# Performance work log

Measured on AMD Instinct MI355X. Metric: run time of the kernel, lower is better.

The kernel has to match this reference:

```python
import jax, jax.numpy as jnp
import numpy as np

N_NODES = 100000
D = 256
N_TYPES = 4
E1 = 300000
E2 = 300000


def setup_inputs() -> dict:
    key = jax.random.key(0)
    ks = jax.random.split(key, 9)
    x = jax.random.normal(ks[0], (N_NODES, D), dtype=jnp.float32)
    hyperedge_index_s1 = jax.random.randint(ks[1], (2, E1 * 1), 0, N_NODES, dtype=jnp.int32)
    hyperedge_type_s1 = jax.random.randint(ks[2], (E1,), 0, N_TYPES, dtype=jnp.int32)
    hyperedge_index_s2 = jax.random.randint(ks[3], (2, E2 * 2), 0, N_NODES, dtype=jnp.int32)
    hyperedge_type_s2 = jax.random.randint(ks[4], (E2,), 0, N_TYPES, dtype=jnp.int32)
    # xavier_normal init for A: std = sqrt(2 / (fan_in + fan_out))
    A_s1 = jax.random.normal(ks[5], (N_TYPES, 1 * D, D), dtype=jnp.float32) * np.sqrt(2.0 / (D + D)).astype(np.float32)
    A_s2 = jax.random.normal(ks[6], (N_TYPES, 2 * D, D), dtype=jnp.float32) * np.sqrt(2.0 / (2 * D + D)).astype(np.float32)
    lim = 1.0 / np.sqrt(D)
    W_c = jax.random.uniform(ks[7], (D, D), minval=-lim, maxval=lim, dtype=jnp.float32)
    b_c = jax.random.uniform(ks[8], (D,), minval=-lim, maxval=lim, dtype=jnp.float32)
    return dict(x=x,
                hyperedge_index_s1=hyperedge_index_s1, hyperedge_type_s1=hyperedge_type_s1,
                hyperedge_index_s2=hyperedge_index_s2, hyperedge_type_s2=hyperedge_type_s2,
                A_s1=A_s1, A_s2=A_s2, W_c=W_c, b_c=b_c)


def _shape_agg(x, A, idx, etype, shape, n_nodes):
    """Per-hyperedge-shape gather -> per-type matmul -> normalize -> scatter-add."""
    d = x.shape[1]
    e = etype.shape[0]
    # concat the `shape` source node features per hyperedge: [E, shape*d]
    src = x[idx[0]].reshape(e, shape * d)
    # first target slot per hyperedge: [E]
    dst = idx[1].reshape(e, shape)[:, 0]
    agg = jnp.zeros((n_nodes, d), dtype=x.dtype)
    for t in range(A.shape[0]):  # small fixed number of edge types
        mask = etype == t
        tmp = src @ A[t]  # [E, d]
        # per-destination count within this (shape, type) group == torch.unique counts
        counts = jax.ops.segment_sum(mask.astype(x.dtype), dst, num_segments=n_nodes)
        norm = jnp.where(mask, 1.0 / jnp.maximum(counts[dst], 1.0), 0.0)
        agg = agg.at[dst].add(norm[:, None] * tmp)
    return agg


def reference(x, hyperedge_index_s1, hyperedge_type_s1,
              hyperedge_index_s2, hyperedge_type_s2,
              A_s1, A_s2, W_c, b_c):
    n = x.shape[0]
    agg = _shape_agg(x, A_s1, hyperedge_index_s1, hyperedge_type_s1, 1, n)
    agg = agg + _shape_agg(x, A_s2, hyperedge_index_s2, hyperedge_type_s2, 2, n)
    return x @ W_c.T + b_c + agg
```

## Files before the change

### kernel.cpp

```cpp
#include <hip/hip_runtime.h>
#include <stdint.h>

#define N_NODES 100000
#define D 256
#define NT 4

typedef float f32x4 __attribute__((ext_vector_type(4)));
typedef __bf16 bf16x8 __attribute__((ext_vector_type(8)));
typedef unsigned int uint32x4 __attribute__((ext_vector_type(4)));
typedef unsigned int uint32x2 __attribute__((ext_vector_type(2)));

__device__ __forceinline__ unsigned short f2bf(float f) {
    unsigned u = __float_as_uint(f);
    u += 0x7FFF + ((u >> 16) & 1);
    return (unsigned short)(u >> 16);
}

__device__ __forceinline__ void gload_lds16(const void* g, void* lds) {
    __builtin_amdgcn_global_load_lds(
        (const __attribute__((address_space(1))) unsigned int*)g,
        (__attribute__((address_space(3))) unsigned int*)lds, 16, 0, 0);
}


__global__ void k_count_both(const int* __restrict__ idx1, const int* __restrict__ ty1, int E1,
                             const int* __restrict__ idx2, const int* __restrict__ ty2, int E2,
                             int* __restrict__ counts) {
    int e = blockIdx.x * 256 + threadIdx.x;
    if (e < E1) {
        int t = ty1[e];
        int dst = idx1[(size_t)E1 + e];
        atomicAdd(&counts[t * N_NODES + dst], 1);
    }
    if (e < E2) {
        int t = ty2[e];
        int dst = idx2[(size_t)2 * E2 + (size_t)2 * e];
        atomicAdd(&counts[NT * N_NODES + t * N_NODES + dst], 1);
    }
}


__global__ __launch_bounds__(256) void k_scan1(const int* __restrict__ in, int n,
        int* __restrict__ outv, int* __restrict__ bsums) {
    __shared__ int s[256];
    int tid = threadIdx.x;
    int i = blockIdx.x * 1024 + tid * 4;
    int v0 = 0, v1 = 0, v2 = 0, v3 = 0;
    if (i + 3 < n) {
        int4 v = *(const int4*)(in + i);
        v0 = v.x; v1 = v.y; v2 = v.z; v3 = v.w;
    } else {
        if (i     < n) v0 = in[i];
        if (i + 1 < n) v1 = in[i + 1];
        if (i + 2 < n) v2 = in[i + 2];
        if (i + 3 < n) v3 = in[i + 3];
    }
    int tsum = v0 + v1 + v2 + v3;
    s[tid] = tsum; __syncthreads();
    for (int off = 1; off < 256; off <<= 1) {
        int t = (tid >= off) ? s[tid - off] : 0;
        __syncthreads();
        s[tid] += t;
        __syncthreads();
    }
    int excl = s[tid] - tsum;
    if (tid == 255) bsums[blockIdx.x] = s[255];
    int o0 = excl, o1 = o0 + v0, o2 = o1 + v1, o3 = o2 + v2;
    if (i + 3 < n) {
        *(int4*)(outv + i) = make_int4(o0, o1, o2, o3);
    } else {
        if (i     < n) outv[i]     = o0;
        if (i + 1 < n) outv[i + 1] = o1;
        if (i + 2 < n) outv[i + 2] = o2;
        if (i + 3 < n) outv[i + 3] = o3;
    }
}

__global__ __launch_bounds__(1024) void k_scan2(int* __restrict__ bsums, int nb) {
    __shared__ int s[1024];
    int t = threadIdx.x;
    int v = (t < nb) ? bsums[t] : 0;
    s[t] = v; __syncthreads();
    for (int off = 1; off < 1024; off <<= 1) {
        int u = (t >= off) ? s[t - off] : 0;
        __syncthreads();
        s[t] += u;
        __syncthreads();
    }
    if (t < nb) bsums[t] = s[t] - v;
}

__global__ __launch_bounds__(256) void k_scan3(int* __restrict__ cellofs,
        int* __restrict__ cellcur, const int* __restrict__ bsums, int n) {
    int i = blockIdx.x * 1024 + threadIdx.x * 4;
    int add = bsums[blockIdx.x];
    if (i + 3 < n) {
        int4 v = *(int4*)(cellofs + i);
        v.x += add; v.y += add; v.z += add; v.w += add;
        *(int4*)(cellofs + i) = v;
        *(int4*)(cellcur + i) = v;
    } else {
        for (int k = 0; k < 4; ++k)
            if (i + k < n) { int v = cellofs[i + k] + add; cellofs[i + k] = v; cellcur[i + k] = v; }
    }
}


__global__ void k_place_both(const int* __restrict__ idx1, const int* __restrict__ ty1, int E1,
                             int* __restrict__ bucket1,
                             const int* __restrict__ idx2, const int* __restrict__ ty2, int E2,
                             int* __restrict__ bucket2,
                             int* __restrict__ cellcur) {
    int e = blockIdx.x * 256 + threadIdx.x;
    if (e < E1) {
        int t = ty1[e];
        int dst = idx1[(size_t)E1 + e];
        int pos = atomicAdd(&cellcur[t * N_NODES + dst], 1);
        bucket1[pos] = e;
    }
    if (e < E2) {
        int t = ty2[e];
        int dst = idx2[(size_t)2 * E2 + (size_t)2 * e];
        int pos = atomicAdd(&cellcur[NT * N_NODES + t * N_NODES + dst], 1) - E1;
        bucket2[pos] = e;
    }
}


__global__ __launch_bounds__(256) void k_cvt(const float* __restrict__ in,
        unsigned short* __restrict__ ob, int n8) {
    int i = blockIdx.x * 256 + threadIdx.x;
    if (i >= n8) return;
    const float4* p = (const float4*)in + (size_t)i * 2;
    float4 v0 = p[0], v1 = p[1];
    union { unsigned short us[8]; uint4 u4; } o;
    o.us[0] = f2bf(v0.x); o.us[1] = f2bf(v0.y); o.us[2] = f2bf(v0.z); o.us[3] = f2bf(v0.w);
    o.us[4] = f2bf(v1.x); o.us[5] = f2bf(v1.y); o.us[6] = f2bf(v1.z); o.us[7] = f2bf(v1.w);
    *(uint4*)(ob + (size_t)i * 8) = o.u4;
}


__global__ void k_cvt_At(const float* __restrict__ A, unsigned short* __restrict__ AT, int K) {
    __shared__ float tl[32][33];
    const float* Ab = A + (size_t)blockIdx.z * K * D;
    unsigned short* Ob = AT + (size_t)blockIdx.z * D * K;
    int k0 = blockIdx.x * 32, j0 = blockIdx.y * 32;
    int lx = threadIdx.x, ly = threadIdx.y;
    for (int yy = ly; yy < 32; yy += 8)
        tl[yy][lx] = Ab[(size_t)(k0 + yy) * D + j0 + lx];
    __syncthreads();
    for (int yy = ly; yy < 32; yy += 8)
        Ob[(size_t)(j0 + yy) * K + k0 + lx] = f2bf(tl[lx][yy]);
}


__global__ __launch_bounds__(256) void k_init_mfma(const unsigned short* __restrict__ xb,
        const unsigned short* __restrict__ Wb, const float* __restrict__ bias,
        float* __restrict__ out, int n) {
    __shared__ __align__(16) char xs[64 * 128];
    int row0 = blockIdx.x * 64;
    int tid = threadIdx.x;
    int lane = tid & 63, w = tid >> 6;
    int l15 = lane & 15, l4 = lane >> 4;
    f32x4 acc[4][4];
    #pragma unroll
    for (int m = 0; m < 4; ++m)
        #pragma unroll
        for (int nn = 0; nn < 4; ++nn) acc[m][nn] = (f32x4)0.f;

    for (int kk = 0; kk < D; kk += 64) {
        #pragma unroll
        for (int it = 0; it < 2; ++it) {
            int f = it * 256 + tid;
            int r = f >> 3, q0 = f & 7;
            int q = q0 ^ (r & 7);
            int gr = row0 + r; if (gr >= n) gr = n - 1;
            gload_lds16(xb + (size_t)gr * D + kk + q * 8, xs + f * 16);
        }
        bf16x8 bfr[2][4];
        #pragma unroll
        for (int ks = 0; ks < 2; ++ks)
            #pragma unroll
            for (int nn = 0; nn < 4; ++nn) {
                int j = w * 64 + nn * 16 + l15;
                int k = kk + ks * 32 + l4 * 8;
                bfr[ks][nn] = *(const bf16x8*)(Wb + (size_t)j * D + k);
            }
        __syncthreads();
        #pragma unroll
        for (int ks = 0; ks < 2; ++ks)
            #pragma unroll
            for (int m = 0; m < 4; ++m) {
                int R = m * 16 + l15;
                int C = ks * 4 + l4;
                bf16x8 a = *(const bf16x8*)(xs + R * 128 + ((C ^ (R & 7)) << 4));
                #pragma unroll
                for (int nn = 0; nn < 4; ++nn)
                    acc[m][nn] = __builtin_amdgcn_mfma_f32_16x16x32_bf16(
                        a, bfr[ks][nn], acc[m][nn], 0, 0, 0);
            }
        __syncthreads();
    }
    #pragma unroll
    for (int m = 0; m < 4; ++m)
        #pragma unroll
        for (int nn = 0; nn < 4; ++nn) {
            int col = w * 64 + nn * 16 + l15;
            float bv = bias[col];
            #pragma unroll
            for (int r = 0; r < 4; ++r) {
                int row = row0 + m * 16 + l4 * 4 + r;
                if (row < n) out[(size_t)row * D + col] = acc[m][nn][r] + bv;
            }
        }
}


template<int SHAPE, int SCR>
__global__ __launch_bounds__(256, 4) void k_edge_mfma(const unsigned short* __restrict__ xb,
        const int* __restrict__ idx, const unsigned short* __restrict__ AT,
        float* __restrict__ out, unsigned short* __restrict__ eo, int E, int rebase,
        const int* __restrict__ counts, const int* __restrict__ cellofs,
        const int* __restrict__ bucket) {
    constexpr int K = SHAPE * 256;
    __shared__ __align__(16) unsigned short re[16][264];
    __shared__ __align__(16) char xs[64 * 128];
    __shared__ int srcS[SHAPE][64];
    __shared__ int dstS[64];
    __shared__ float normS[64];

    int t = blockIdx.y;
    int offs_t = cellofs[t * N_NODES] - rebase;
    int end_t = (t == NT - 1) ? E : cellofs[(t + 1) * N_NODES] - rebase;
    int cnt = end_t - offs_t;
    int tile = blockIdx.x * 64;
    if (tile >= cnt) return;
    int nE = min(64, cnt - tile);
    int base = offs_t + tile;
    int tid = threadIdx.x;

    if (tid < 64) {
        bool valid = tid < nE;
        int e = bucket[base + (valid ? tid : 0)];
        int dst = idx[(size_t)SHAPE * E + (size_t)SHAPE * e];
        dstS[tid] = dst;
        int c = counts[t * N_NODES + dst];
        normS[tid] = valid ? 1.0f / (float)(c > 1 ? c : 1) : 0.0f;
        srcS[0][tid] = idx[SHAPE * e];
        if (SHAPE == 2) srcS[SHAPE - 1][tid] = idx[SHAPE * e + SHAPE - 1];
    }
    __syncthreads();

    const unsigned short* Bt = AT + (size_t)t * D * K;
    int lane = tid & 63, w = tid >> 6;
    int l15 = lane & 15, l4 = lane >> 4;
    f32x4 acc[4][4];
    #pragma unroll
    for (int m = 0; m < 4; ++m)
        #pragma unroll
        for (int nn = 0; nn < 4; ++nn) acc[m][nn] = (f32x4)0.f;

    for (int kk = 0; kk < K; kk += 64) {
        #pragma unroll
        for (int it = 0; it < 2; ++it) {
            int f = it * 256 + tid;
            int r = f >> 3, q0 = f & 7;
            int q = q0 ^ (r & 7);
            int node = srcS[SHAPE == 2 ? (kk >> 8) : 0][r];
            int col = (kk & 255) + q * 8;
            gload_lds16(xb + (size_t)node * D + col, xs + f * 16);
        }
        bf16x8 bfr[2][4];
        #pragma unroll
        for (int ks = 0; ks < 2; ++ks)
            #pragma unroll
            for (int nn = 0; nn < 4; ++nn) {
                int j = w * 64 + nn * 16 + l15;
                int k = kk + ks * 32 + l4 * 8;
                bfr[ks][nn] = *(const bf16x8*)(Bt + (size_t)j * K + k);
            }
        __syncthreads();
        #pragma unroll
        for (int ks = 0; ks < 2; ++ks)
            #pragma unroll
            for (int m = 0; m < 4; ++m) {
                int R = m * 16 + l15;
                int C = ks * 4 + l4;
                bf16x8 a = *(const bf16x8*)(xs + R * 128 + ((C ^ (R & 7)) << 4));
                #pragma unroll
                for (int nn = 0; nn < 4; ++nn)
                    acc[m][nn] = __builtin_amdgcn_mfma_f32_16x16x32_bf16(
                        a, bfr[ks][nn], acc[m][nn], 0, 0, 0);
            }
        __syncthreads();
    }

    if constexpr (SCR) {
        #pragma unroll
        for (int q = 0; q < 4; ++q) {
            __syncthreads();
            #pragma unroll
            for (int r = 0; r < 4; ++r) {
                int rl = l4 * 4 + r;
                float nm = normS[q * 16 + rl];
                #pragma unroll
                for (int nn = 0; nn < 4; ++nn) {
                    int col = w * 64 + nn * 16 + l15;
                    re[rl][col] = f2bf(nm * acc[q][nn][r]);
                }
            }
            __syncthreads();
            #pragma unroll
            for (int it = 0; it < 2; ++it) {
                int f = it * 256 + tid;
                int row = f >> 5, seg = f & 31;
                int grow = q * 16 + row;
                if (grow < nE) {
                    uint32x4 v = *(const uint32x4*)&re[row][seg * 8];
                    *(uint32x4*)(eo + (size_t)(base + grow) * D + seg * 8) = v;
                }
            }
        }
    } else {
        #pragma unroll
        for (int m = 0; m < 4; ++m)
            #pragma unroll
            for (int r = 0; r < 4; ++r) {
                int rr = m * 16 + l4 * 4 + r;
                if (rr < nE) {
                    float nm = normS[rr];
                    size_t ob = (size_t)dstS[rr] * D;
                    #pragma unroll
                    for (int nn = 0; nn < 4; ++nn) {
                        int col = w * 64 + nn * 16 + l15;
                        atomicAdd(&out[ob + col], nm * acc[m][nn][r]);
                    }
                }
            }
    }
}


__device__ __forceinline__ void acc_runs(const unsigned short* __restrict__ eo,
        const int* __restrict__ counts, const int* __restrict__ cellofs, int rebase,
        int dst, int lane, float& a0, float& a1, float& a2, float& a3, int& tot) {
    #pragma unroll
    for (int t = 0; t < NT; ++t) {
        int start = cellofs[t * N_NODES + dst] - rebase;
        int c = counts[t * N_NODES + dst];
        tot += c;
        for (int i = 0; i < c; ++i) {
            const uint32x2* row = (const uint32x2*)(eo + (size_t)(start + i) * D + lane * 4);
            uint32x2 v = __builtin_nontemporal_load(row);
            a0 += __uint_as_float(v.x << 16);
            a1 += __uint_as_float(v.x & 0xFFFF0000u);
            a2 += __uint_as_float(v.y << 16);
            a3 += __uint_as_float(v.y & 0xFFFF0000u);
        }
    }
}

__global__ __launch_bounds__(256) void k_reduce_one(const unsigned short* __restrict__ eo,
        const int* __restrict__ counts, const int* __restrict__ cellofs, int rebase,
        float* __restrict__ out) {
    int wv = threadIdx.x >> 6, lane = threadIdx.x & 63;
    int dst = blockIdx.x * 4 + wv;
    if (dst >= N_NODES) return;
    float a0 = 0.f, a1 = 0.f, a2 = 0.f, a3 = 0.f;
    int tot = 0;
    acc_runs(eo, counts, cellofs, rebase, dst, lane, a0, a1, a2, a3, tot);
    if (tot) {
        float4* o = (float4*)&out[(size_t)dst * D + lane * 4];
        float4 cur = *o;
        cur.x += a0; cur.y += a1; cur.z += a2; cur.w += a3;
        *o = cur;
    }
}

__global__ __launch_bounds__(256) void k_reduce_two(
        const unsigned short* __restrict__ eo1, const int* __restrict__ c1,
        const int* __restrict__ o1,
        const unsigned short* __restrict__ eo2, const int* __restrict__ c2,
        const int* __restrict__ o2, int rb2,
        float* __restrict__ out) {
    int wv = threadIdx.x >> 6, lane = threadIdx.x & 63;
    int dst = blockIdx.x * 4 + wv;
    if (dst >= N_NODES) return;
    float a0 = 0.f, a1 = 0.f, a2 = 0.f, a3 = 0.f;
    int tot = 0;
    acc_runs(eo1, c1, o1, 0, dst, lane, a0, a1, a2, a3, tot);
    acc_runs(eo2, c2, o2, rb2, dst, lane, a0, a1, a2, a3, tot);
    if (tot) {
        float4* o = (float4*)&out[(size_t)dst * D + lane * 4];
        float4 cur = *o;
        cur.x += a0; cur.y += a1; cur.z += a2; cur.w += a3;
        *o = cur;
    }
}


extern "C" void kernel_launch(void* const* d_in, const int* in_sizes, int n_in,
                              void* d_out, int out_size, void* d_ws, size_t ws_size,
                              hipStream_t stream) {
    const float* x  = (const float*)d_in[0];
    const int* idx1 = (const int*)d_in[1];
    const int* ty1  = (const int*)d_in[2];
    const int* idx2 = (const int*)d_in[3];
    const int* ty2  = (const int*)d_in[4];
    const float* A1 = (const float*)d_in[5];
    const float* A2 = (const float*)d_in[6];
    const float* W  = (const float*)d_in[7];
    const float* b  = (const float*)d_in[8];
    float* out = (float*)d_out;

    int E1 = in_sizes[2];
    int E2 = in_sizes[4];
    int maxE = E1 > E2 ? E1 : E2;
    const int NCELL = NT * N_NODES;
    const int NC2 = 2 * NCELL;
    const int NB2 = (NC2 + 1023) / 1024;
    const int NRB = (N_NODES + 3) / 4;

    char* p = (char*)d_ws;
    unsigned short* xb  = (unsigned short*)p; p += (size_t)N_NODES * D * 2;
    unsigned short* Wb  = (unsigned short*)p; p += (size_t)D * D * 2;
    unsigned short* A1T = (unsigned short*)p; p += (size_t)NT * D * 256 * 2;
    unsigned short* A2T = (unsigned short*)p; p += (size_t)NT * D * 512 * 2;
    int* counts  = (int*)p; p += (size_t)NC2 * 4;
    int* cellofs = (int*)p; p += (size_t)NC2 * 4;
    int* cellcur = (int*)p; p += (size_t)NC2 * 4;
    int* bsums   = (int*)p; p += 1024 * 4;
    int* bucket1 = (int*)p; p += (size_t)maxE * 4;
    int* bucket2 = (int*)p; p += (size_t)maxE * 4;
    unsigned short* eo1 = (unsigned short*)p; p += (size_t)maxE * D * 2;
    unsigned short* eo2 = (unsigned short*)p; p += (size_t)maxE * D * 2;
    size_t need2 = (size_t)(p - (char*)d_ws);
    int mode = (need2 <= ws_size) ? 2 : 0;
    int* counts2  = counts + NCELL;
    int* cellofs2 = cellofs + NCELL;

    k_cvt<<<(N_NODES * D / 8 + 255) / 256, 256, 0, stream>>>(x, xb, N_NODES * D / 8);
    k_cvt<<<(D * D / 8 + 255) / 256, 256, 0, stream>>>(W, Wb, D * D / 8);
    k_cvt_At<<<dim3(256 / 32, D / 32, NT), dim3(32, 8), 0, stream>>>(A1, A1T, 256);
    k_cvt_At<<<dim3(512 / 32, D / 32, NT), dim3(32, 8), 0, stream>>>(A2, A2T, 512);

    k_init_mfma<<<(N_NODES + 63) / 64, 256, 0, stream>>>(xb, Wb, b, out, N_NODES);

    hipMemsetAsync(counts, 0, (size_t)NC2 * sizeof(int), stream);
    k_count_both<<<(maxE + 255) / 256, 256, 0, stream>>>(idx1, ty1, E1, idx2, ty2, E2, counts);
    k_scan1<<<NB2, 256, 0, stream>>>(counts, NC2, cellofs, bsums);
    k_scan2<<<1, 1024, 0, stream>>>(bsums, NB2);
    k_scan3<<<NB2, 256, 0, stream>>>(cellofs, cellcur, bsums, NC2);
    k_place_both<<<(maxE + 255) / 256, 256, 0, stream>>>(idx1, ty1, E1, bucket1,
                                                          idx2, ty2, E2, bucket2, cellcur);

    if (mode == 2) {
        k_edge_mfma<1, 1><<<dim3((E1 + 63) / 64, NT), 256, 0, stream>>>(
            xb, idx1, A1T, out, eo1, E1, 0, counts, cellofs, bucket1);
        k_edge_mfma<2, 1><<<dim3((E2 + 63) / 64, NT), 256, 0, stream>>>(
            xb, idx2, A2T, out, eo2, E2, E1, counts2, cellofs2, bucket2);
        k_reduce_two<<<NRB, 256, 0, stream>>>(eo1, counts, cellofs,
                                              eo2, counts2, cellofs2, E1, out);
    } else {
        k_edge_mfma<1, 0><<<dim3((E1 + 63) / 64, NT), 256, 0, stream>>>(
            xb, idx1, A1T, out, nullptr, E1, 0, counts, cellofs, bucket1);
        k_edge_mfma<2, 0><<<dim3((E2 + 63) / 64, NT), 256, 0, stream>>>(
            xb, idx2, A2T, out, nullptr, E2, E1, counts2, cellofs2, bucket2);
    }
}
```

Baseline: 573.7 us.

## Order edge tiles by source node and scatter outputs to destination-sorted slots

Adds a second counting sort keyed by (type, source node), so the edge MFMA kernels process edges grouped by source. This is meant to improve cache locality of the gathered x rows. Each edge's output row is written to its destination-sorted position through a new epos array, so the segmented reduction is unchanged. The cost is doubled count/scan/place work, more atomics, a larger scan, and scattered rather than contiguous writes of edge outputs.

```diff
diff --git a/kernel.cpp b/kernel.cpp
--- a/kernel.cpp
+++ b/kernel.cpp
@@ -23,19 +23,20 @@
 }
 
 
-__global__ void k_count_both(const int* __restrict__ idx1, const int* __restrict__ ty1, int E1,
-                             const int* __restrict__ idx2, const int* __restrict__ ty2, int E2,
-                             int* __restrict__ counts) {
+__global__ void k_count_all(const int* __restrict__ idx1, const int* __restrict__ ty1, int E1,
+                            const int* __restrict__ idx2, const int* __restrict__ ty2, int E2,
+                            int* __restrict__ counts) {
+    const int NC = NT * N_NODES;
     int e = blockIdx.x * 256 + threadIdx.x;
     if (e < E1) {
         int t = ty1[e];
-        int dst = idx1[(size_t)E1 + e];
-        atomicAdd(&counts[t * N_NODES + dst], 1);
+        atomicAdd(&counts[t * N_NODES + idx1[(size_t)E1 + e]], 1);
+        atomicAdd(&counts[2 * NC + t * N_NODES + idx1[e]], 1);
     }
     if (e < E2) {
         int t = ty2[e];
-        int dst = idx2[(size_t)2 * E2 + (size_t)2 * e];
-        atomicAdd(&counts[NT * N_NODES + t * N_NODES + dst], 1);
+        atomicAdd(&counts[NC + t * N_NODES + idx2[(size_t)2 * E2 + (size_t)2 * e]], 1);
+        atomicAdd(&counts[3 * NC + t * N_NODES + idx2[(size_t)2 * e]], 1);
     }
 }
 
@@ -79,15 +80,19 @@
 __global__ __launch_bounds__(1024) void k_scan2(int* __restrict__ bsums, int nb) {
     __shared__ int s[1024];
     int t = threadIdx.x;
-    int v = (t < nb) ? bsums[t] : 0;
-    s[t] = v; __syncthreads();
+    int v0 = (2 * t     < nb) ? bsums[2 * t]     : 0;
+    int v1 = (2 * t + 1 < nb) ? bsums[2 * t + 1] : 0;
+    int tsum = v0 + v1;
+    s[t] = tsum; __syncthreads();
     for (int off = 1; off < 1024; off <<= 1) {
         int u = (t >= off) ? s[t - off] : 0;
         __syncthreads();
         s[t] += u;
         __syncthreads();
     }
-    if (t < nb) bsums[t] = s[t] - v;
+    int excl = s[t] - tsum;
+    if (2 * t     < nb) bsums[2 * t]     = excl;
+    if (2 * t + 1 < nb) bsums[2 * t + 1] = excl + v0;
 }
 
 __global__ __launch_bounds__(256) void k_scan3(int* __restrict__ cellofs,
@@ -106,23 +111,28 @@
 }
 
 
-__global__ void k_place_both(const int* __restrict__ idx1, const int* __restrict__ ty1, int E1,
-                             int* __restrict__ bucket1,
-                             const int* __restrict__ idx2, const int* __restrict__ ty2, int E2,
-                             int* __restrict__ bucket2,
-                             int* __restrict__ cellcur) {
+__global__ void k_place_all(const int* __restrict__ idx1, const int* __restrict__ ty1, int E1,
+                            int* __restrict__ epos1, int* __restrict__ bucketS1,
+                            const int* __restrict__ idx2, const int* __restrict__ ty2, int E2,
+                            int* __restrict__ epos2, int* __restrict__ bucketS2,
+                            int* __restrict__ cellcur) {
+    const int NC = NT * N_NODES;
     int e = blockIdx.x * 256 + threadIdx.x;
     if (e < E1) {
         int t = ty1[e];
         int dst = idx1[(size_t)E1 + e];
-        int pos = atomicAdd(&cellcur[t * N_NODES + dst], 1);
-        bucket1[pos] = e;
+        int src = idx1[e];
+        epos1[e] = atomicAdd(&cellcur[t * N_NODES + dst], 1);
+        int ps = atomicAdd(&cellcur[2 * NC + t * N_NODES + src], 1) - (E1 + E2);
+        bucketS1[ps] = e;
     }
     if (e < E2) {
         int t = ty2[e];
         int dst = idx2[(size_t)2 * E2 + (size_t)2 * e];
-        int pos = atomicAdd(&cellcur[NT * N_NODES + t * N_NODES + dst], 1) - E1;
-        bucket2[pos] = e;
+        int src = idx2[(size_t)2 * e];
+        epos2[e] = atomicAdd(&cellcur[NC + t * N_NODES + dst], 1) - E1;
+        int ps = atomicAdd(&cellcur[3 * NC + t * N_NODES + src], 1) - (2 * E1 + E2);
+        bucketS2[ps] = e;
     }
 }
 
@@ -219,19 +229,20 @@
 template<int SHAPE, int SCR>
 __global__ __launch_bounds__(256, 4) void k_edge_mfma(const unsigned short* __restrict__ xb,
         const int* __restrict__ idx, const unsigned short* __restrict__ AT,
-        float* __restrict__ out, unsigned short* __restrict__ eo, int E, int rebase,
-        const int* __restrict__ counts, const int* __restrict__ cellofs,
-        const int* __restrict__ bucket) {
+        float* __restrict__ out, unsigned short* __restrict__ eo, int E,
+        const int* __restrict__ countsD, const int* __restrict__ cellofsS, int rebaseS,
+        const int* __restrict__ bucketS, const int* __restrict__ epos) {
     constexpr int K = SHAPE * 256;
     __shared__ __align__(16) unsigned short re[16][264];
     __shared__ __align__(16) char xs[64 * 128];
     __shared__ int srcS[SHAPE][64];
     __shared__ int dstS[64];
+    __shared__ int eposS[64];
     __shared__ float normS[64];
 
     int t = blockIdx.y;
-    int offs_t = cellofs[t * N_NODES] - rebase;
-    int end_t = (t == NT - 1) ? E : cellofs[(t + 1) * N_NODES] - rebase;
+    int offs_t = cellofsS[t * N_NODES] - rebaseS;
+    int end_t = (t == NT - 1) ? E : cellofsS[(t + 1) * N_NODES] - rebaseS;
     int cnt = end_t - offs_t;
     int tile = blockIdx.x * 64;
     if (tile >= cnt) return;
@@ -241,10 +252,11 @@
 
     if (tid < 64) {
         bool valid = tid < nE;
-        int e = bucket[base + (valid ? tid : 0)];
+        int e = bucketS[base + (valid ? tid : 0)];
         int dst = idx[(size_t)SHAPE * E + (size_t)SHAPE * e];
         dstS[tid] = dst;
-        int c = counts[t * N_NODES + dst];
+        eposS[tid] = epos[e];
+        int c = countsD[t * N_NODES + dst];
         normS[tid] = valid ? 1.0f / (float)(c > 1 ? c : 1) : 0.0f;
         srcS[0][tid] = idx[SHAPE * e];
         if (SHAPE == 2) srcS[SHAPE - 1][tid] = idx[SHAPE * e + SHAPE - 1];
@@ -317,7 +329,7 @@
                 int grow = q * 16 + row;
                 if (grow < nE) {
                     uint32x4 v = *(const uint32x4*)&re[row][seg * 8];
-                    *(uint32x4*)(eo + (size_t)(base + grow) * D + seg * 8) = v;
+                    *(uint32x4*)(eo + (size_t)eposS[grow] * D + seg * 8) = v;
                 }
             }
         }
@@ -357,23 +369,6 @@
             a2 += __uint_as_float(v.y << 16);
             a3 += __uint_as_float(v.y & 0xFFFF0000u);
         }
-    }
-}
-
-__global__ __launch_bounds__(256) void k_reduce_one(const unsigned short* __restrict__ eo,
-        const int* __restrict__ counts, const int* __restrict__ cellofs, int rebase,
-        float* __restrict__ out) {
-    int wv = threadIdx.x >> 6, lane = threadIdx.x & 63;
-    int dst = blockIdx.x * 4 + wv;
-    if (dst >= N_NODES) return;
-    float a0 = 0.f, a1 = 0.f, a2 = 0.f, a3 = 0.f;
-    int tot = 0;
-    acc_runs(eo, counts, cellofs, rebase, dst, lane, a0, a1, a2, a3, tot);
-    if (tot) {
-        float4* o = (float4*)&out[(size_t)dst * D + lane * 4];
-        float4 cur = *o;
-        cur.x += a0; cur.y += a1; cur.z += a2; cur.w += a3;
-        *o = cur;
     }
 }
 
@@ -417,8 +412,8 @@
     int E2 = in_sizes[4];
     int maxE = E1 > E2 ? E1 : E2;
     const int NCELL = NT * N_NODES;
-    const int NC2 = 2 * NCELL;
-    const int NB2 = (NC2 + 1023) / 1024;
+    const int NC4 = 4 * NCELL;
+    const int NB4 = (NC4 + 1023) / 1024;
     const int NRB = (N_NODES + 3) / 4;
 
     char* p = (char*)d_ws;
@@ -426,18 +421,22 @@
     unsigned short* Wb  = (unsigned short*)p; p += (size_t)D * D * 2;
     unsigned short* A1T = (unsigned short*)p; p += (size_t)NT * D * 256 * 2;
     unsigned short* A2T = (unsigned short*)p; p += (size_t)NT * D * 512 * 2;
-    int* counts  = (int*)p; p += (size_t)NC2 * 4;
-    int* cellofs = (int*)p; p += (size_t)NC2 * 4;
-    int* cellcur = (int*)p; p += (size_t)NC2 * 4;
-    int* bsums   = (int*)p; p += 1024 * 4;
-    int* bucket1 = (int*)p; p += (size_t)maxE * 4;
-    int* bucket2 = (int*)p; p += (size_t)maxE * 4;
+    int* counts  = (int*)p; p += (size_t)NC4 * 4;
+    int* cellofs = (int*)p; p += (size_t)NC4 * 4;
+    int* cellcur = (int*)p; p += (size_t)NC4 * 4;
+    int* bsums   = (int*)p; p += 2048 * 4;
+    int* epos1   = (int*)p; p += (size_t)maxE * 4;
+    int* epos2   = (int*)p; p += (size_t)maxE * 4;
+    int* bucketS1= (int*)p; p += (size_t)maxE * 4;
+    int* bucketS2= (int*)p; p += (size_t)maxE * 4;
     unsigned short* eo1 = (unsigned short*)p; p += (size_t)maxE * D * 2;
     unsigned short* eo2 = (unsigned short*)p; p += (size_t)maxE * D * 2;
     size_t need2 = (size_t)(p - (char*)d_ws);
     int mode = (need2 <= ws_size) ? 2 : 0;
-    int* counts2  = counts + NCELL;
-    int* cellofs2 = cellofs + NCELL;
+    int* countsD2  = counts + NCELL;
+    int* cellofsD2 = cellofs + NCELL;
+    const int rbS1 = E1 + E2;
+    const int rbS2 = 2 * E1 + E2;
 
     k_cvt<<<(N_NODES * D / 8 + 255) / 256, 256, 0, stream>>>(x, xb, N_NODES * D / 8);
     k_cvt<<<(D * D / 8 + 255) / 256, 256, 0, stream>>>(W, Wb, D * D / 8);
@@ -446,25 +445,29 @@
 
     k_init_mfma<<<(N_NODES + 63) / 64, 256, 0, stream>>>(xb, Wb, b, out, N_NODES);
 
-    hipMemsetAsync(counts, 0, (size_t)NC2 * sizeof(int), stream);
-    k_count_both<<<(maxE + 255) / 256, 256, 0, stream>>>(idx1, ty1, E1, idx2, ty2, E2, counts);
-    k_scan1<<<NB2, 256, 0, stream>>>(counts, NC2, cellofs, bsums);
-    k_scan2<<<1, 1024, 0, stream>>>(bsums, NB2);
-    k_scan3<<<NB2, 256, 0, stream>>>(cellofs, cellcur, bsums, NC2);
-    k_place_both<<<(maxE + 255) / 256, 256, 0, stream>>>(idx1, ty1, E1, bucket1,
-                                                          idx2, ty2, E2, bucket2, cellcur);
+    hipMemsetAsync(counts, 0, (size_t)NC4 * sizeof(int), stream);
+    k_count_all<<<(maxE + 255) / 256, 256, 0, stream>>>(idx1, ty1, E1, idx2, ty2, E2, counts);
+    k_scan1<<<NB4, 256, 0, stream>>>(counts, NC4, cellofs, bsums);
+    k_scan2<<<1, 1024, 0, stream>>>(bsums, NB4);
+    k_scan3<<<NB4, 256, 0, stream>>>(cellofs, cellcur, bsums, NC4);
+    k_place_all<<<(maxE + 255) / 256, 256, 0, stream>>>(idx1, ty1, E1, epos1, bucketS1,
+                                                        idx2, ty2, E2, epos2, bucketS2, cellcur);
 
     if (mode == 2) {
         k_edge_mfma<1, 1><<<dim3((E1 + 63) / 64, NT), 256, 0, stream>>>(
-            xb, idx1, A1T, out, eo1, E1, 0, counts, cellofs, bucket1);
+            xb, idx1, A1T, out, eo1, E1,
+            counts, cellofs + 2 * NCELL, rbS1, bucketS1, epos1);
         k_edge_mfma<2, 1><<<dim3((E2 + 63) / 64, NT), 256, 0, stream>>>(
-            xb, idx2, A2T, out, eo2, E2, E1, counts2, cellofs2, bucket2);
+            xb, idx2, A2T, out, eo2, E2,
+            countsD2, cellofs + 3 * NCELL, rbS2, bucketS2, epos2);
         k_reduce_two<<<NRB, 256, 0, stream>>>(eo1, counts, cellofs,
-                                              eo2, counts2, cellofs2, E1, out);
+                                              eo2, countsD2, cellofsD2, E1, out);
     } else {
         k_edge_mfma<1, 0><<<dim3((E1 + 63) / 64, NT), 256, 0, stream>>>(
-            xb, idx1, A1T, out, nullptr, E1, 0, counts, cellofs, bucket1);
+            xb, idx1, A1T, out, nullptr, E1,
+            counts, cellofs + 2 * NCELL, rbS1, bucketS1, epos1);
         k_edge_mfma<2, 0><<<dim3((E2 + 63) / 64, NT), 256, 0, stream>>>(
-            xb, idx2, A2T, out, nullptr, E2, E1, counts2, cellofs2, bucket2);
-    }
-}
+            xb, idx2, A2T, out, nullptr, E2,
+            countsD2, cellofs + 3 * NCELL, rbS2, bucketS2, epos2);
+    }
+}
```

New measurement: 636.0 us. 1.11x slower.
